# Kernel tuning notes

Hardware: AMD Instinct MI355X
Metric: run time of the kernel (lower is better)

## Reference

```python
import jax, jax.numpy as jnp
import numpy as np


def _cdist(p1, p2):
    # Euclidean cdist via the matmul expansion (matches torch.cdist p=2 fast path):
    # ||a-b||^2 = ||a||^2 + ||b||^2 - 2 a.b ; clamp tiny negatives before sqrt.
    sq1 = jnp.sum(p1 * p1, axis=-1, keepdims=True)        # (N, 1)
    sq2 = jnp.sum(p2 * p2, axis=-1, keepdims=True).T      # (1, M)
    d2 = sq1 + sq2 - 2.0 * (p1 @ p2.T)                    # (N, M)
    return jnp.sqrt(jnp.maximum(d2, 0.0))


def setup_inputs() -> dict:
    key = jax.random.key(0)
    k1, k2 = jax.random.split(key)
    N, M = 16384, 16384
    points1 = jax.random.normal(k1, (N, 3), dtype=jnp.float32)
    points2 = jax.random.normal(k2, (M, 3), dtype=jnp.float32)
    return {"points1": points1, "points2": points2}


def reference(points1, points2):
    dist = _cdist(points1, points2)                        # (N, M)
    min1 = jnp.min(dist, axis=1)                           # (N,) nearest in points2
    min2 = jnp.min(dist, axis=0)                           # (M,) nearest in points1
    return jnp.sum(min1) + jnp.sum(min2)
```

## Files before the change

kernel.cpp:

```cpp
#include <hip/hip_runtime.h>
#include <math.h>


typedef _Float16 half8    __attribute__((ext_vector_type(8)));
typedef float    floatx16 __attribute__((ext_vector_type(16)));

constexpr int NPTS = 16384;
constexpr int HALF = 8192;
constexpr int ROWS = 128;
constexpr int BLK  = 1024;

__device__ __forceinline__ uint2 pack_point(const float* __restrict__ P, int j)
{
    float x = P[3*j], y = P[3*j+1], z = P[3*j+2];
    _Float16 hx = (_Float16)x, hy = (_Float16)y, hz = (_Float16)z;
    float qx = (float)hx, qy = (float)hy, qz = (float)hz;
    _Float16 hw = (_Float16)(qx*qx + qy*qy + qz*qz);
    union { _Float16 h[4]; uint2 u; } p;
    p.h[0] = hx; p.h[1] = hy; p.h[2] = hz; p.h[3] = hw;
    return p.u;
}

__global__ __launch_bounds__(BLK, 8) void chamfer_sweep_kernel(
    const float* __restrict__ P1, const float* __restrict__ P2,
    float* __restrict__ part, int n1, int n2)
{
    __shared__ uint2 sB[HALF];
    __shared__ float sRowMin[4][ROWS];

    const int dir   = blockIdx.z;
    const int half  = blockIdx.y;
    const float* PA = dir == 0 ? P1 : P2;
    const float* PB = dir == 0 ? P2 : P1;
    const int nA    = dir == 0 ? n1 : n2;
    const int nB    = dir == 0 ? n2 : n1;

    const int tid  = threadIdx.x;
    const int wave = tid >> 6;
    const int lane = tid & 63;
    const int n    = lane & 31;
    const int g    = lane >> 5;
    const bool g0  = (g == 0);
    const int wr   = wave & 3;
    const int wq   = wave >> 2;

    for (int j = tid; j < HALF; j += BLK) {
        int jg = half * HALF + j;
        int jj = jg < nB ? jg : nB - 1;
        sB[j] = pack_point(PB, jj);
    }

    const _Float16 h0 = (_Float16)0.0f;
    half8 af;
    {
        int arow = blockIdx.x * ROWS + wr * 32 + n;
        int j = arow < nA ? arow : nA - 1;
        union { uint2 u; _Float16 h[4]; } au; au.u = pack_point(PA, j);
        const _Float16 m2 = (_Float16)(-2.0f);
        af[0] = g0 ? (_Float16)(au.h[0] * m2) : h0;
        af[1] = g0 ? (_Float16)(au.h[1] * m2) : h0;
        af[2] = g0 ? (_Float16)(au.h[2] * m2) : h0;
        af[3] = g0 ? (_Float16)1.0f : h0;
        af[4] = g0 ? au.h[3] : h0;
        af[5] = h0; af[6] = h0; af[7] = h0;
    }

    __syncthreads();

    floatx16 rowmin;
#pragma unroll
    for (int r = 0; r < 16; ++r) rowmin[r] = 1e30f;
    const floatx16 zacc = {};

    union BF { half8 v; unsigned u[4]; uint2 lo; };
    BF bu0, bu1;
    { union { _Float16 h[2]; unsigned u; } q;
      q.h[0] = (_Float16)1.0f; q.h[1] = h0;
      bu0.u[2] = q.u; bu0.u[3] = 0u;
      bu1.u[2] = q.u; bu1.u[3] = 0u; }

    constexpr int QLEN = HALF >> 2;
    constexpr int NT   = QLEN / 64;
    const uint2* qbase = sB + wq * QLEN + n;
    for (int bt = 0; bt < NT; ++bt) {
        const uint2* p = qbase + bt * 64;
        bu0.lo = p[0];
        bu1.lo = p[32];

        floatx16 d = __builtin_amdgcn_mfma_f32_32x32x16_f16(af, bu0.v, zacc, 0, 0, 0);
#pragma unroll
        for (int r = 0; r < 16; ++r) rowmin[r] = fminf(rowmin[r], d[r]);

        d = __builtin_amdgcn_mfma_f32_32x32x16_f16(af, bu1.v, zacc, 0, 0, 0);
#pragma unroll
        for (int r = 0; r < 16; ++r) rowmin[r] = fminf(rowmin[r], d[r]);
    }

#pragma unroll
    for (int mask = 1; mask <= 16; mask <<= 1)
#pragma unroll
        for (int r = 0; r < 16; ++r)
            rowmin[r] = fminf(rowmin[r], __shfl_xor(rowmin[r], mask));

    if (n == 0) {
#pragma unroll
        for (int r = 0; r < 16; ++r) {
            int rr = wr * 32 + g * 4 + ((r & 3) + 8 * (r >> 2));
            sRowMin[wq][rr] = rowmin[r];
        }
    }
    __syncthreads();

    if (tid < ROWS) {
        float m = fminf(fminf(sRowMin[0][tid], sRowMin[1][tid]),
                        fminf(sRowMin[2][tid], sRowMin[3][tid]));
        int grow = blockIdx.x * ROWS + tid;
        if (grow < nA)
            part[(size_t)(((dir << 14) + grow) << 1) + half] = m;
    }
}

__global__ __launch_bounds__(256) void reduce_kernel(
    const float* __restrict__ part, float* __restrict__ out,
    int n1, int n2)
{
    __shared__ float s[256];
    int rr = blockIdx.x * 256 + threadIdx.x;
    int dir = rr >> 14, row = rr & 16383;
    float acc = 0.0f;
    if (row < (dir == 0 ? n1 : n2)) {
        const float2 v = ((const float2*)part)[rr];
        acc = sqrtf(fmaxf(fminf(v.x, v.y), 0.0f));
    }
    s[threadIdx.x] = acc;
    __syncthreads();
    for (int w = 128; w > 0; w >>= 1) {
        if (threadIdx.x < w) s[threadIdx.x] += s[threadIdx.x + w];
        __syncthreads();
    }
    if (threadIdx.x == 0) atomicAdd(out, s[0]);
}

extern "C" void kernel_launch(void* const* d_in, const int* in_sizes, int n_in,
                              void* d_out, int out_size, void* d_ws, size_t ws_size,
                              hipStream_t stream) {
    const float* P1 = (const float*)d_in[0];
    const float* P2 = (const float*)d_in[1];
    const int n1 = in_sizes[0] / 3;
    const int n2 = in_sizes[1] / 3;
    float* part = (float*)d_ws;
    float* out  = (float*)d_out;

    hipMemsetAsync(out, 0, sizeof(float), stream);

    {
        dim3 grid(NPTS / ROWS, 2, 2);
        chamfer_sweep_kernel<<<grid, BLK, 0, stream>>>(P1, P2, part, n1, n2);
    }
    reduce_kernel<<<(2 * NPTS) / 256, 256, 0, stream>>>(part, out, n1, n2);
}
```

Measured before the change: 81.24 us.

## Register-tile two A fragments per wave and store prebuilt B fragments in LDS

Each wave now covers 64 rows with two A fragments, and every B fragment it loads feeds two MFMAs, so LDS reads per MFMA are halved. Rows per block double to 256. B points are staged in LDS as complete 16-byte f16 fragments, with the constant 1 already in place, so no per-iteration register assembly is needed. The trade-off is twice the LDS footprint (128KB per block), half as many blocks (one per CU), more accumulator registers and a larger unrolled loop, which may limit latency hiding.

```diff
diff --git a/kernel.cpp b/kernel.cpp
--- a/kernel.cpp
+++ b/kernel.cpp
@@ -7,7 +7,7 @@
 
 constexpr int NPTS = 16384;
 constexpr int HALF = 8192;
-constexpr int ROWS = 128;
+constexpr int ROWS = 256;
 constexpr int BLK  = 1024;
 
 __device__ __forceinline__ uint2 pack_point(const float* __restrict__ P, int j)
@@ -21,11 +21,24 @@
     return p.u;
 }
 
-__global__ __launch_bounds__(BLK, 8) void chamfer_sweep_kernel(
+__device__ __forceinline__ uint4 pack_frag16(const float* __restrict__ P, int j)
+{
+    float x = P[3*j], y = P[3*j+1], z = P[3*j+2];
+    _Float16 hx = (_Float16)x, hy = (_Float16)y, hz = (_Float16)z;
+    float qx = (float)hx, qy = (float)hy, qz = (float)hz;
+    _Float16 hw = (_Float16)(qx*qx + qy*qy + qz*qz);
+    union { _Float16 h[8]; uint4 u; } f;
+    f.h[0] = hx; f.h[1] = hy; f.h[2] = hz; f.h[3] = hw;
+    f.h[4] = (_Float16)1.0f;
+    f.h[5] = (_Float16)0.0f; f.h[6] = (_Float16)0.0f; f.h[7] = (_Float16)0.0f;
+    return f.u;
+}
+
+__global__ __launch_bounds__(BLK, 4) void chamfer_sweep_kernel(
     const float* __restrict__ P1, const float* __restrict__ P2,
     float* __restrict__ part, int n1, int n2)
 {
-    __shared__ uint2 sB[HALF];
+    __shared__ uint4 sB[HALF];
     __shared__ float sRowMin[4][ROWS];
 
     const int dir   = blockIdx.z;
@@ -41,72 +54,79 @@
     const int n    = lane & 31;
     const int g    = lane >> 5;
     const bool g0  = (g == 0);
-    const int wr   = wave & 3;
-    const int wq   = wave >> 2;
+    const int rgp  = wave & 3;
+    const int bq   = wave >> 2;
 
     for (int j = tid; j < HALF; j += BLK) {
         int jg = half * HALF + j;
         int jj = jg < nB ? jg : nB - 1;
-        sB[j] = pack_point(PB, jj);
+        sB[j] = pack_frag16(PB, jj);
     }
 
     const _Float16 h0 = (_Float16)0.0f;
-    half8 af;
+    const _Float16 m2 = (_Float16)(-2.0f);
+    half8 af0, af1;
     {
-        int arow = blockIdx.x * ROWS + wr * 32 + n;
-        int j = arow < nA ? arow : nA - 1;
-        union { uint2 u; _Float16 h[4]; } au; au.u = pack_point(PA, j);
-        const _Float16 m2 = (_Float16)(-2.0f);
-        af[0] = g0 ? (_Float16)(au.h[0] * m2) : h0;
-        af[1] = g0 ? (_Float16)(au.h[1] * m2) : h0;
-        af[2] = g0 ? (_Float16)(au.h[2] * m2) : h0;
-        af[3] = g0 ? (_Float16)1.0f : h0;
-        af[4] = g0 ? au.h[3] : h0;
-        af[5] = h0; af[6] = h0; af[7] = h0;
+        int abase = blockIdx.x * ROWS + rgp * 64 + n;
+        int j0 = abase      < nA ? abase      : nA - 1;
+        int j1 = abase + 32 < nA ? abase + 32 : nA - 1;
+        union { uint2 u; _Float16 h[4]; } a0, a1;
+        a0.u = pack_point(PA, j0);
+        a1.u = pack_point(PA, j1);
+        af0[0] = g0 ? (_Float16)(a0.h[0] * m2) : h0;
+        af0[1] = g0 ? (_Float16)(a0.h[1] * m2) : h0;
+        af0[2] = g0 ? (_Float16)(a0.h[2] * m2) : h0;
+        af0[3] = g0 ? (_Float16)1.0f : h0;
+        af0[4] = g0 ? a0.h[3] : h0;
+        af0[5] = h0; af0[6] = h0; af0[7] = h0;
+        af1[0] = g0 ? (_Float16)(a1.h[0] * m2) : h0;
+        af1[1] = g0 ? (_Float16)(a1.h[1] * m2) : h0;
+        af1[2] = g0 ? (_Float16)(a1.h[2] * m2) : h0;
+        af1[3] = g0 ? (_Float16)1.0f : h0;
+        af1[4] = g0 ? a1.h[3] : h0;
+        af1[5] = h0; af1[6] = h0; af1[7] = h0;
     }
 
     __syncthreads();
 
-    floatx16 rowmin;
+    floatx16 rowmin0, rowmin1;
 #pragma unroll
-    for (int r = 0; r < 16; ++r) rowmin[r] = 1e30f;
+    for (int r = 0; r < 16; ++r) { rowmin0[r] = 1e30f; rowmin1[r] = 1e30f; }
     const floatx16 zacc = {};
 
-    union BF { half8 v; unsigned u[4]; uint2 lo; };
-    BF bu0, bu1;
-    { union { _Float16 h[2]; unsigned u; } q;
-      q.h[0] = (_Float16)1.0f; q.h[1] = h0;
-      bu0.u[2] = q.u; bu0.u[3] = 0u;
-      bu1.u[2] = q.u; bu1.u[3] = 0u; }
+    const half8* qb = (const half8*)sB + bq * 2048 + n;
+#pragma unroll 8
+    for (int it = 0; it < 32; ++it) {
+        half8 B0 = qb[it * 64];
+        half8 B1 = qb[it * 64 + 32];
 
-    constexpr int QLEN = HALF >> 2;
-    constexpr int NT   = QLEN / 64;
-    const uint2* qbase = sB + wq * QLEN + n;
-    for (int bt = 0; bt < NT; ++bt) {
-        const uint2* p = qbase + bt * 64;
-        bu0.lo = p[0];
-        bu1.lo = p[32];
+        floatx16 dA = __builtin_amdgcn_mfma_f32_32x32x16_f16(af0, B0, zacc, 0, 0, 0);
+        floatx16 dB = __builtin_amdgcn_mfma_f32_32x32x16_f16(af0, B1, zacc, 0, 0, 0);
+#pragma unroll
+        for (int r = 0; r < 16; ++r)
+            rowmin0[r] = fminf(fminf(rowmin0[r], dA[r]), dB[r]);
 
-        floatx16 d = __builtin_amdgcn_mfma_f32_32x32x16_f16(af, bu0.v, zacc, 0, 0, 0);
+        dA = __builtin_amdgcn_mfma_f32_32x32x16_f16(af1, B0, zacc, 0, 0, 0);
+        dB = __builtin_amdgcn_mfma_f32_32x32x16_f16(af1, B1, zacc, 0, 0, 0);
 #pragma unroll
-        for (int r = 0; r < 16; ++r) rowmin[r] = fminf(rowmin[r], d[r]);
-
-        d = __builtin_amdgcn_mfma_f32_32x32x16_f16(af, bu1.v, zacc, 0, 0, 0);
-#pragma unroll
-        for (int r = 0; r < 16; ++r) rowmin[r] = fminf(rowmin[r], d[r]);
+        for (int r = 0; r < 16; ++r)
+            rowmin1[r] = fminf(fminf(rowmin1[r], dA[r]), dB[r]);
     }
 
 #pragma unroll
     for (int mask = 1; mask <= 16; mask <<= 1)
 #pragma unroll
-        for (int r = 0; r < 16; ++r)
-            rowmin[r] = fminf(rowmin[r], __shfl_xor(rowmin[r], mask));
+        for (int r = 0; r < 16; ++r) {
+            rowmin0[r] = fminf(rowmin0[r], __shfl_xor(rowmin0[r], mask));
+            rowmin1[r] = fminf(rowmin1[r], __shfl_xor(rowmin1[r], mask));
+        }
 
     if (n == 0) {
 #pragma unroll
         for (int r = 0; r < 16; ++r) {
-            int rr = wr * 32 + g * 4 + ((r & 3) + 8 * (r >> 2));
-            sRowMin[wq][rr] = rowmin[r];
+            int rr = rgp * 64 + g * 4 + ((r & 3) + 8 * (r >> 2));
+            sRowMin[bq][rr]      = rowmin0[r];
+            sRowMin[bq][rr + 32] = rowmin1[r];
         }
     }
     __syncthreads();
```

Result: slower. 102.6 us (+26.3%).

## Compute distance matrix once and derive both row and column minima symmetrically

Applied to the files above, without the earlier changes.

The two directional sweeps, which each built the full N×M distance tile set, are replaced by one pass over the matrix. From each MFMA output tile it takes row minima in registers and column minima through a cross-half shuffle plus shared-memory integer atomicMin, then merges both into global buffers with integer atomicMin. This halves the MFMA work but adds per-tile column reductions, LDS atomics, global atomics, and a single-block final reduce. The integer atomicMin on float bits assumes the values are non-negative, and negative squared distances from rounding could break that ordering.

```diff
diff --git a/kernel.cpp b/kernel.cpp
--- a/kernel.cpp
+++ b/kernel.cpp
@@ -5,10 +5,10 @@
 typedef _Float16 half8    __attribute__((ext_vector_type(8)));
 typedef float    floatx16 __attribute__((ext_vector_type(16)));
 
-constexpr int NPTS = 16384;
-constexpr int HALF = 8192;
-constexpr int ROWS = 128;
-constexpr int BLK  = 1024;
+constexpr int NPTS  = 16384;
+constexpr int SEG   = 2048;
+constexpr int AROWS = 512;
+constexpr int BLK   = 1024;
 
 __device__ __forceinline__ uint2 pack_point(const float* __restrict__ P, int j)
 {
@@ -21,19 +21,25 @@
     return p.u;
 }
 
-__global__ __launch_bounds__(BLK, 8) void chamfer_sweep_kernel(
+__device__ __forceinline__ uint4 pack_frag16(const float* __restrict__ P, int j)
+{
+    float x = P[3*j], y = P[3*j+1], z = P[3*j+2];
+    _Float16 hx = (_Float16)x, hy = (_Float16)y, hz = (_Float16)z;
+    float qx = (float)hx, qy = (float)hy, qz = (float)hz;
+    _Float16 hw = (_Float16)(qx*qx + qy*qy + qz*qz);
+    union { _Float16 h[8]; uint4 u; } f;
+    f.h[0] = hx; f.h[1] = hy; f.h[2] = hz; f.h[3] = hw;
+    f.h[4] = (_Float16)1.0f;
+    f.h[5] = (_Float16)0.0f; f.h[6] = (_Float16)0.0f; f.h[7] = (_Float16)0.0f;
+    return f.u;
+}
+
+__global__ __launch_bounds__(BLK, 4) void chamfer_sym_kernel(
     const float* __restrict__ P1, const float* __restrict__ P2,
-    float* __restrict__ part, int n1, int n2)
+    int* __restrict__ rowmin, int* __restrict__ colmin, int n1, int n2)
 {
-    __shared__ uint2 sB[HALF];
-    __shared__ float sRowMin[4][ROWS];
-
-    const int dir   = blockIdx.z;
-    const int half  = blockIdx.y;
-    const float* PA = dir == 0 ? P1 : P2;
-    const float* PB = dir == 0 ? P2 : P1;
-    const int nA    = dir == 0 ? n1 : n2;
-    const int nB    = dir == 0 ? n2 : n1;
+    __shared__ uint4 sB[SEG];
+    __shared__ int   sColMin[SEG];
 
     const int tid  = threadIdx.x;
     const int wave = tid >> 6;
@@ -41,21 +47,21 @@
     const int n    = lane & 31;
     const int g    = lane >> 5;
     const bool g0  = (g == 0);
-    const int wr   = wave & 3;
-    const int wq   = wave >> 2;
 
-    for (int j = tid; j < HALF; j += BLK) {
-        int jg = half * HALF + j;
-        int jj = jg < nB ? jg : nB - 1;
-        sB[j] = pack_point(PB, jj);
+    const int cbase = blockIdx.y * SEG;
+    for (int j = tid; j < SEG; j += BLK) {
+        sColMin[j] = 0x7F7F7F7F;
+        int jj = cbase + j;
+        if (jj >= n2) jj = n2 - 1;
+        sB[j] = pack_frag16(P2, jj);
     }
 
     const _Float16 h0 = (_Float16)0.0f;
     half8 af;
     {
-        int arow = blockIdx.x * ROWS + wr * 32 + n;
-        int j = arow < nA ? arow : nA - 1;
-        union { uint2 u; _Float16 h[4]; } au; au.u = pack_point(PA, j);
+        int arow = blockIdx.x * AROWS + wave * 32 + n;
+        int j = arow < n1 ? arow : n1 - 1;
+        union { uint2 u; _Float16 h[4]; } au; au.u = pack_point(P1, j);
         const _Float16 m2 = (_Float16)(-2.0f);
         af[0] = g0 ? (_Float16)(au.h[0] * m2) : h0;
         af[1] = g0 ? (_Float16)(au.h[1] * m2) : h0;
@@ -67,78 +73,81 @@
 
     __syncthreads();
 
-    floatx16 rowmin;
+    floatx16 rmin;
 #pragma unroll
-    for (int r = 0; r < 16; ++r) rowmin[r] = 1e30f;
+    for (int r = 0; r < 16; ++r) rmin[r] = 1e30f;
     const floatx16 zacc = {};
 
-    union BF { half8 v; unsigned u[4]; uint2 lo; };
-    BF bu0, bu1;
-    { union { _Float16 h[2]; unsigned u; } q;
-      q.h[0] = (_Float16)1.0f; q.h[1] = h0;
-      bu0.u[2] = q.u; bu0.u[3] = 0u;
-      bu1.u[2] = q.u; bu1.u[3] = 0u; }
+    const half8* qb = (const half8*)sB + n;
+#pragma unroll 2
+    for (int t = 0; t < SEG / 64; ++t) {
+        half8 B0 = qb[t * 64];
+        half8 B1 = qb[t * 64 + 32];
 
-    constexpr int QLEN = HALF >> 2;
-    constexpr int NT   = QLEN / 64;
-    const uint2* qbase = sB + wq * QLEN + n;
-    for (int bt = 0; bt < NT; ++bt) {
-        const uint2* p = qbase + bt * 64;
-        bu0.lo = p[0];
-        bu1.lo = p[32];
+        floatx16 dA = __builtin_amdgcn_mfma_f32_32x32x16_f16(af, B0, zacc, 0, 0, 0);
+        floatx16 dB = __builtin_amdgcn_mfma_f32_32x32x16_f16(af, B1, zacc, 0, 0, 0);
 
-        floatx16 d = __builtin_amdgcn_mfma_f32_32x32x16_f16(af, bu0.v, zacc, 0, 0, 0);
 #pragma unroll
-        for (int r = 0; r < 16; ++r) rowmin[r] = fminf(rowmin[r], d[r]);
+        for (int r = 0; r < 16; ++r)
+            rmin[r] = fminf(fminf(rmin[r], dA[r]), dB[r]);
 
-        d = __builtin_amdgcn_mfma_f32_32x32x16_f16(af, bu1.v, zacc, 0, 0, 0);
+        float cA = dA[0], cB = dB[0];
 #pragma unroll
-        for (int r = 0; r < 16; ++r) rowmin[r] = fminf(rowmin[r], d[r]);
+        for (int r = 1; r + 1 < 16; r += 2) {
+            cA = fminf(fminf(cA, dA[r]), dA[r + 1]);
+            cB = fminf(fminf(cB, dB[r]), dB[r + 1]);
+        }
+        cA = fminf(cA, dA[15]);
+        cB = fminf(cB, dB[15]);
+        cA = fminf(cA, __shfl_xor(cA, 32));
+        cB = fminf(cB, __shfl_xor(cB, 32));
+        if (g0) {
+            atomicMin(&sColMin[t * 64 + n],      __float_as_int(cA));
+            atomicMin(&sColMin[t * 64 + 32 + n], __float_as_int(cB));
+        }
     }
 
 #pragma unroll
     for (int mask = 1; mask <= 16; mask <<= 1)
 #pragma unroll
         for (int r = 0; r < 16; ++r)
-            rowmin[r] = fminf(rowmin[r], __shfl_xor(rowmin[r], mask));
+            rmin[r] = fminf(rmin[r], __shfl_xor(rmin[r], mask));
 
     if (n == 0) {
+        int rbase = blockIdx.x * AROWS + wave * 32 + g * 4;
 #pragma unroll
         for (int r = 0; r < 16; ++r) {
-            int rr = wr * 32 + g * 4 + ((r & 3) + 8 * (r >> 2));
-            sRowMin[wq][rr] = rowmin[r];
+            int row = rbase + (r & 3) + 8 * (r >> 2);
+            if (row < n1)
+                atomicMin(&rowmin[row], __float_as_int(rmin[r]));
         }
     }
+
     __syncthreads();
-
-    if (tid < ROWS) {
-        float m = fminf(fminf(sRowMin[0][tid], sRowMin[1][tid]),
-                        fminf(sRowMin[2][tid], sRowMin[3][tid]));
-        int grow = blockIdx.x * ROWS + tid;
-        if (grow < nA)
-            part[(size_t)(((dir << 14) + grow) << 1) + half] = m;
+    for (int j = tid; j < SEG; j += BLK) {
+        int c = cbase + j;
+        if (c < n2) atomicMin(&colmin[c], sColMin[j]);
     }
 }
 
-__global__ __launch_bounds__(256) void reduce_kernel(
-    const float* __restrict__ part, float* __restrict__ out,
-    int n1, int n2)
+__global__ __launch_bounds__(1024) void reduce_kernel(
+    const int* __restrict__ mins, float* __restrict__ out, int n1, int n2)
 {
-    __shared__ float s[256];
-    int rr = blockIdx.x * 256 + threadIdx.x;
-    int dir = rr >> 14, row = rr & 16383;
+    __shared__ float s[1024];
     float acc = 0.0f;
-    if (row < (dir == 0 ? n1 : n2)) {
-        const float2 v = ((const float2*)part)[rr];
-        acc = sqrtf(fmaxf(fminf(v.x, v.y), 0.0f));
+    for (int j = threadIdx.x; j < 2 * NPTS; j += 1024) {
+        bool isrow = j < NPTS;
+        int idx = isrow ? j : j - NPTS;
+        if (idx < (isrow ? n1 : n2))
+            acc += sqrtf(fmaxf(__int_as_float(mins[j]), 0.0f));
     }
     s[threadIdx.x] = acc;
     __syncthreads();
-    for (int w = 128; w > 0; w >>= 1) {
+    for (int w = 512; w > 0; w >>= 1) {
         if (threadIdx.x < w) s[threadIdx.x] += s[threadIdx.x + w];
         __syncthreads();
     }
-    if (threadIdx.x == 0) atomicAdd(out, s[0]);
+    if (threadIdx.x == 0) out[0] = s[0];
 }
 
 extern "C" void kernel_launch(void* const* d_in, const int* in_sizes, int n_in,
@@ -148,14 +157,16 @@
     const float* P2 = (const float*)d_in[1];
     const int n1 = in_sizes[0] / 3;
     const int n2 = in_sizes[1] / 3;
-    float* part = (float*)d_ws;
+
+    int* rowmin = (int*)d_ws;
+    int* colmin = rowmin + NPTS;
     float* out  = (float*)d_out;
 
-    hipMemsetAsync(out, 0, sizeof(float), stream);
+    hipMemsetAsync(d_ws, 0x7F, 2 * NPTS * sizeof(int), stream);
 
     {
-        dim3 grid(NPTS / ROWS, 2, 2);
-        chamfer_sweep_kernel<<<grid, BLK, 0, stream>>>(P1, P2, part, n1, n2);
+        dim3 grid(NPTS / AROWS, NPTS / SEG);
+        chamfer_sym_kernel<<<grid, BLK, 0, stream>>>(P1, P2, rowmin, colmin, n1, n2);
     }
-    reduce_kernel<<<(2 * NPTS) / 256, 256, 0, stream>>>(part, out, n1, n2);
+    reduce_kernel<<<1, 1024, 0, stream>>>(rowmin, out, n1, n2);
 }
```

After: 90.46 us. 1.11x slower.
